# Kernel tuning notes

Hardware: AMD Instinct MI355X
Metric: run time of the kernel (lower is better)

Reference implementation:

```python
import jax, jax.numpy as jnp
from jax import lax
import numpy as np

B, H, W, D_MODEL = 2, 64, 64, 192
D_INNER, D_STATE, DT_RANK = 384, 16, 12
L = H * W
LN_EPS = 1e-5


def setup_inputs() -> dict:
    ks = jax.random.split(jax.random.key(0), 12)
    rng = np.random.default_rng(0)
    perm = rng.permutation(L).astype(np.int32)

    def p(i, shape, scale=0.02):
        return jax.random.normal(ks[i], shape, dtype=jnp.float32) * scale

    return {
        "x": jax.random.normal(ks[0], (B, H, W, D_MODEL), dtype=jnp.float32),
        "condition": jax.random.normal(ks[1], (B, H, W, D_MODEL), dtype=jnp.float32),
        "W_in": p(2, (2 * D_INNER, D_MODEL)),
        "W_con": p(3, (D_INNER, D_MODEL)),
        "conv_w": p(4, (D_INNER, 1, 3, 3)),
        "conv_b": jnp.zeros((D_INNER,), jnp.float32),
        "con_conv_w": p(5, (D_INNER, 1, 3, 3)),
        "con_conv_b": jnp.zeros((D_INNER,), jnp.float32),
        "x_proj_w": p(6, (DT_RANK + 2 * D_STATE, D_INNER)),
        "dt_proj_w": p(7, (D_INNER, DT_RANK)),
        "dt_proj_b": p(8, (D_INNER,), 0.1),
        "A_logs": jnp.tile(jnp.log(jnp.arange(1, D_STATE + 1, dtype=jnp.float32))[None, :], (D_INNER, 1)),
        "Ds": jnp.ones((D_INNER,), jnp.float32),
        "ln_w": jnp.ones((D_INNER,), jnp.float32),
        "ln_b": jnp.zeros((D_INNER,), jnp.float32),
        "W_out": p(9, (D_MODEL, D_INNER)),
        "scan_path": jnp.asarray(perm),
        "rev_scan_path": jnp.asarray(np.argsort(perm).astype(np.int32)),
    }


def _dwconv(x, w, b):
    # depthwise 3x3 conv, SAME padding; x: [B, C, H, W], w: [C, 1, 3, 3]
    y = lax.conv_general_dilated(x, w, (1, 1), "SAME",
                                 dimension_numbers=("NCHW", "OIHW", "NCHW"),
                                 feature_group_count=x.shape[1])
    return y + b[None, :, None, None]


def _selective_scan(u, delta, A, Bs, Cs, D):
    # u, delta: [B, D, L]; A: [D, N]; Bs, Cs: [B, N, L]; D: [D]
    dA = jnp.exp(jnp.einsum("bdl,dn->lbdn", delta, A))          # [L, B, D, N]
    dBu = jnp.einsum("bdl,bnl,bdl->lbdn", delta, Bs, u)          # [L, B, D, N]
    Ct = jnp.transpose(Cs, (2, 0, 1))                             # [L, B, N]
    h0 = jnp.zeros(dA.shape[1:], dA.dtype)

    def step(h, inp):
        a, b, c = inp
        h = a * h + b
        return h, jnp.einsum("bdn,bn->bd", h, c)

    _, ys = lax.scan(step, h0, (dA, dBu, Ct))                     # ys: [L, B, D]
    y = jnp.transpose(ys, (1, 2, 0))                              # [B, D, L]
    return y + u * D[None, :, None]


def _forward(x, condition, W_in, W_con, conv_w, conv_b, con_conv_w, con_conv_b,
             x_proj_w, dt_proj_w, dt_proj_b, A_logs, Ds, ln_w, ln_b, W_out,
             scan_path, rev_scan_path):
    b, h, w, _ = x.shape
    l = h * w
    xz = x @ W_in.T                                               # [B, H, W, 2*Din]
    xa, z = jnp.split(xz, 2, axis=-1)
    z = jax.nn.silu(z)
    c = condition @ W_con.T
    xa = jax.nn.silu(_dwconv(jnp.transpose(xa, (0, 3, 1, 2)), conv_w, conv_b))
    c = jax.nn.silu(_dwconv(jnp.transpose(c, (0, 3, 1, 2)), con_conv_w, con_conv_b))
    d = xa.shape[1]
    xs = xa.reshape(b, d, l)[:, :, scan_path]                     # forward_permutation, K=1
    cs = c.reshape(b, d, l)[:, :, scan_path]
    x_dbl = jnp.einsum("bdl,cd->bcl", xs + cs, x_proj_w)          # [B, R+2N, L]
    r, n = dt_proj_w.shape[1], A_logs.shape[1]
    dts = jnp.einsum("brl,dr->bdl", x_dbl[:, :r], dt_proj_w)
    Bs = x_dbl[:, r:r + n]
    Cs = x_dbl[:, r + n:]
    A = -jnp.exp(A_logs)
    delta = jax.nn.softplus(dts + dt_proj_b[None, :, None])       # delta_softplus=True
    y = _selective_scan(xs, delta, A, Bs, Cs, Ds)                 # [B, D, L]
    y = y[:, :, rev_scan_path]                                    # backward_permutation
    y = jnp.transpose(y, (0, 2, 1))                               # [B, L, D]
    mu = jnp.mean(y, axis=-1, keepdims=True)
    var = jnp.var(y, axis=-1, keepdims=True)
    y = (y - mu) * lax.rsqrt(var + LN_EPS) * ln_w + ln_b          # out_norm
    y = y.reshape(b, h, w, d) * z
    return y @ W_out.T                                            # out_proj (no bias)


def reference(x, condition, W_in, W_con, conv_w, conv_b, con_conv_w, con_conv_b,
              x_proj_w, dt_proj_w, dt_proj_b, A_logs, Ds, ln_w, ln_b, W_out,
              scan_path, rev_scan_path):
    return _forward(x, condition, W_in, W_con, conv_w, conv_b, con_conv_w,
                    con_conv_b, x_proj_w, dt_proj_w, dt_proj_b, A_logs, Ds,
                    ln_w, ln_b, W_out, scan_path, rev_scan_path)
```

## Files before the change

### kernel.cpp

```cpp
#include <hip/hip_runtime.h>
#include <math.h>

#define BB 2
#define HH 64
#define WW 64
#define DM 192
#define DI 384
#define NS 16
#define DTR 12
#define LL 4096
#define ROWS (BB*LL)
#define NCHUNK 64
#define LCHUNK 64
#define NCOMB 448

typedef __attribute__((ext_vector_type(8))) short bf16x8;
typedef __attribute__((ext_vector_type(4))) float f32x4;

__device__ __forceinline__ float silu_f(float v) {
    return v / (1.0f + __expf(-v));
}

__device__ __forceinline__ unsigned short f2bf(float f) {
    union { float f; unsigned int u; } c; c.f = f;
    unsigned int u = c.u;
    u += 0x7fffu + ((u >> 16) & 1u);
    return (unsigned short)(u >> 16);
}

__global__ __launch_bounds__(256) void cast_bf16(
    const float* __restrict__ in, unsigned short* __restrict__ out, int n4)
{
    int i = blockIdx.x * 256 + threadIdx.x;
    if (i >= n4) return;
    float4 v = ((const float4*)in)[i];
    ushort4 o;
    o.x = f2bf(v.x); o.y = f2bf(v.y); o.z = f2bf(v.z); o.w = f2bf(v.w);
    ((ushort4*)out)[i] = o;
}

__global__ __launch_bounds__(256) void cast_weights(
    const float* __restrict__ w_in, const float* __restrict__ w_con,
    const float* __restrict__ w_out,
    unsigned short* __restrict__ w_in_bf, unsigned short* __restrict__ w_con_bf,
    unsigned short* __restrict__ w_out_bf)
{
    int i = blockIdx.x * 256 + threadIdx.x;
    if (i >= 73728) return;
    const float4* src; ushort4* dst; int off;
    if (i < 36864)      { src = (const float4*)w_in;  dst = (ushort4*)w_in_bf;  off = i; }
    else if (i < 55296) { src = (const float4*)w_con; dst = (ushort4*)w_con_bf; off = i - 36864; }
    else                { src = (const float4*)w_out; dst = (ushort4*)w_out_bf; off = i - 55296; }
    float4 v = src[off];
    ushort4 o;
    o.x = f2bf(v.x); o.y = f2bf(v.y); o.z = f2bf(v.z); o.w = f2bf(v.w);
    dst[off] = o;
}

__global__ __launch_bounds__(256) void make_wcomb(
    const float* __restrict__ x_proj_w,
    const float* __restrict__ dt_w,
    unsigned short* __restrict__ wc)
{
    int idx = blockIdx.x * 256 + threadIdx.x;
    if (idx >= NCOMB * DI) return;
    int row = idx / DI, k = idx - row * DI;
    float v = 0.f;
    if (row < 384) {
        const float* dw = dt_w + row * DTR;
        #pragma unroll
        for (int r = 0; r < DTR; ++r) v += dw[r] * x_proj_w[r * DI + k];
    } else if (row < 416) {
        v = x_proj_w[(12 + (row - 384)) * DI + k];
    }
    wc[idx] = f2bf(v);
}

__device__ __forceinline__ void gemm_epilogue(
    int mode, int row, int col, int N, float v,
    const float* __restrict__ bias,
    float* __restrict__ out0, float* __restrict__ out1)
{
    if (mode == 0) {
        if (col < 384) out0[(size_t)row * 384 + col] = v;
        else           out1[(size_t)row * 384 + (col - 384)] = silu_f(v);
    } else if (mode == 1) {
        out0[(size_t)row * N + col] = v;
    } else {
        if (col < 384) {
            float a = v + bias[col];
            out0[(size_t)row * 384 + col] = (a > 20.f) ? a : log1pf(__expf(a));
        } else if (col < 416) {
            int idx = col - 384;
            int pos = (idx < 16) ? ((idx & 7) * 4 + (idx >> 3))
                                 : (((idx - 16) & 7) * 4 + 2 + ((idx - 16) >> 3));
            out1[(size_t)row * 32 + pos] = v;
        }
    }
}

__global__ __launch_bounds__(256) void gemm_bf16(
    const unsigned short* __restrict__ A, const unsigned short* __restrict__ W,
    const float* __restrict__ bias,
    float* __restrict__ out0, float* __restrict__ out1,
    int M, int N, int K, int mode)
{
    __shared__ __align__(16) unsigned short sA[64 * 40];
    __shared__ __align__(16) unsigned short sB[64 * 40];
    const int bm = blockIdx.x * 64;
    const int bn = blockIdx.y * 64;
    const int tid  = threadIdx.x;
    const int wave = tid >> 6;
    const int lane = tid & 63;
    const int quad = lane >> 4;
    const int l16  = lane & 15;

    const int lrow = tid >> 2;
    const int lkof = (tid & 3) * 8;

    f32x4 acc[4];
    #pragma unroll
    for (int t = 0; t < 4; ++t) acc[t] = (f32x4)(0.f);

    const int arow = (wave * 16 + l16) * 40 + quad * 8;

    for (int k0 = 0; k0 < K; k0 += 32) {
        *(bf16x8*)&sA[lrow * 40 + lkof] =
            *(const bf16x8*)&A[(size_t)(bm + lrow) * K + k0 + lkof];
        *(bf16x8*)&sB[lrow * 40 + lkof] =
            *(const bf16x8*)&W[(size_t)(bn + lrow) * K + k0 + lkof];
        __syncthreads();
        bf16x8 a = *(bf16x8*)&sA[arow];
        #pragma unroll
        for (int t = 0; t < 4; ++t) {
            bf16x8 b = *(bf16x8*)&sB[(t * 16 + l16) * 40 + quad * 8];
            acc[t] = __builtin_amdgcn_mfma_f32_16x16x32_bf16(a, b, acc[t], 0, 0, 0);
        }
        __syncthreads();
    }

    #pragma unroll
    for (int t = 0; t < 4; ++t) {
        int col = bn + t * 16 + l16;
        #pragma unroll
        for (int r = 0; r < 4; ++r) {
            int row = bm + wave * 16 + quad * 4 + r;
            gemm_epilogue(mode, row, col, N, acc[t][r], bias, out0, out1);
        }
    }
}

__global__ __launch_bounds__(256) void dwconv2_scatter(
    const float* __restrict__ xin, const float* __restrict__ cin,
    const float* __restrict__ wx, const float* __restrict__ bx,
    const float* __restrict__ wc, const float* __restrict__ bc,
    const int* __restrict__ rev_scan_path,
    float* __restrict__ xs_buf, unsigned short* __restrict__ s_bf)
{
    const int tile = blockIdx.x;
    const int c0   = blockIdx.y * 64;
    const int b    = blockIdx.z;
    const int h0 = (tile >> 3) * 8, w0 = (tile & 7) * 8;
    __shared__ float smx[10 * 10 * 64];
    __shared__ float smc[10 * 10 * 64];
    __shared__ int   jtile[64];

    for (int idx = threadIdx.x; idx < 6400; idx += 256) {
        int pix = idx >> 6, ch = idx & 63;
        int py = pix / 10, px = pix - py * 10;
        int gh = h0 + py - 1, gw = w0 + px - 1;
        float vx = 0.f, vc = 0.f;
        if (gh >= 0 && gh < 64 && gw >= 0 && gw < 64) {
            size_t g = ((size_t)(b * LL + gh * 64 + gw)) * DI + c0 + ch;
            vx = xin[g]; vc = cin[g];
        }
        smx[idx] = vx; smc[idx] = vc;
    }
    if (threadIdx.x < 64) {
        int l = (h0 + (threadIdx.x >> 3)) * 64 + (w0 + (threadIdx.x & 7));
        jtile[threadIdx.x] = rev_scan_path[l];
    }
    __syncthreads();

    const int ch = threadIdx.x & 63;
    const int pq = threadIdx.x >> 6;
    float wrx[9], wrc[9];
    #pragma unroll
    for (int k = 0; k < 9; ++k) {
        wrx[k] = wx[(c0 + ch) * 9 + k];
        wrc[k] = wc[(c0 + ch) * 9 + k];
    }
    const float bvx = bx[c0 + ch];
    const float bvc = bc[c0 + ch];

    #pragma unroll
    for (int i = 0; i < 16; ++i) {
        int p  = pq * 16 + i;
        int ph = p >> 3, pw = p & 7;
        float ax = bvx, ac = bvc;
        #pragma unroll
        for (int ki = 0; ki < 3; ++ki)
            #pragma unroll
            for (int kj = 0; kj < 3; ++kj) {
                int si = ((ph + ki) * 10 + (pw + kj)) * 64 + ch;
                ax += wrx[ki * 3 + kj] * smx[si];
                ac += wrc[ki * 3 + kj] * smc[si];
            }
        float xv = silu_f(ax);
        float sv = xv + silu_f(ac);
        size_t o = ((size_t)(b * LL + jtile[p])) * DI + c0 + ch;
        xs_buf[o] = xv;
        s_bf[o]   = f2bf(sv);
    }
}

__global__ __launch_bounds__(256) void scan_chunkA(
    const float* __restrict__ xs, const float* __restrict__ delta,
    const float* __restrict__ btct, const float* __restrict__ A_logs,
    float* __restrict__ chunkA, float* __restrict__ chunkB)
{
    const int c = blockIdx.x;
    const int g = blockIdx.y;
    const int b = blockIdx.z;
    const int t = threadIdx.x;
    const int grp = t >> 3, p = t & 7;
    const int d = g * 32 + grp;
    const float Av0 = -__expf(A_logs[d * NS + p]);
    const float Av1 = -__expf(A_logs[d * NS + p + 8]);
    const int j0 = c * LCHUNK;

    const float*  dl = delta + ((size_t)b * LL + j0) * DI + d;
    const float*  ul = xs    + ((size_t)b * LL + j0) * DI + d;
    const float2* bl = (const float2*)btct + ((size_t)b * LL + j0) * 16 + p * 2;

    float h0 = 0.f, h1 = 0.f, P0 = 1.f, P1 = 1.f;
    float dv[4], uv[4]; float2 bv[4];
    #pragma unroll
    for (int q = 0; q < 4; ++q) {
        dv[q] = dl[(size_t)q * DI]; uv[q] = ul[(size_t)q * DI]; bv[q] = bl[(size_t)q * 16];
    }
    for (int j = 0; j < LCHUNK; j += 4) {
        float nd[4], nu[4]; float2 nb[4];
        if (j + 4 < LCHUNK) {
            #pragma unroll
            for (int q = 0; q < 4; ++q) {
                int jj = j + 4 + q;
                nd[q] = dl[(size_t)jj * DI]; nu[q] = ul[(size_t)jj * DI]; nb[q] = bl[(size_t)jj * 16];
            }
        }
        #pragma unroll
        for (int q = 0; q < 4; ++q) {
            float e0 = __expf(dv[q] * Av0);
            float e1 = __expf(dv[q] * Av1);
            float du = dv[q] * uv[q];
            h0 = e0 * h0 + bv[q].x * du;
            h1 = e1 * h1 + bv[q].y * du;
            P0 *= e0; P1 *= e1;
        }
        #pragma unroll
        for (int q = 0; q < 4; ++q) { dv[q]=nd[q]; uv[q]=nu[q]; bv[q]=nb[q]; }
    }
    size_t idx = (((size_t)c * BB + b) * DI + d) * 8 + p;
    ((float2*)chunkA)[idx] = make_float2(P0, P1);
    ((float2*)chunkB)[idx] = make_float2(h0, h1);
}

__global__ __launch_bounds__(256) void scan_combine(
    const float* __restrict__ chunkA, const float* __restrict__ chunkB,
    float* __restrict__ hstart)
{
    const int gid = blockIdx.x * 256 + threadIdx.x;
    const size_t stride = (size_t)BB * DI * NS;
    float h = 0.f;
    float a = chunkA[gid], bv = chunkB[gid];
    for (int c = 0; c < NCHUNK; ++c) {
        float na = 0.f, nb = 0.f;
        if (c + 1 < NCHUNK) {
            na = chunkA[(size_t)(c + 1) * stride + gid];
            nb = chunkB[(size_t)(c + 1) * stride + gid];
        }
        hstart[(size_t)c * stride + gid] = h;
        h = a * h + bv;
        a = na; bv = nb;
    }
}

__global__ __launch_bounds__(256) void scan_chunkC(
    const float* __restrict__ xs, const float* __restrict__ delta,
    const float* __restrict__ btct,
    const float* __restrict__ A_logs, const float* __restrict__ Ds,
    const float* __restrict__ hstart,
    float* __restrict__ yt)
{
    const int c = blockIdx.x;
    const int g = blockIdx.y;
    const int b = blockIdx.z;
    const int t = threadIdx.x;
    const int grp = t >> 3, p = t & 7;
    const int d = g * 32 + grp;
    const float Av0 = -__expf(A_logs[d * NS + p]);
    const float Av1 = -__expf(A_logs[d * NS + p + 8]);
    const float Dv = Ds[d];
    const int j0 = c * LCHUNK;

    const float*  dl  = delta + ((size_t)b * LL + j0) * DI + d;
    const float*  ul  = xs    + ((size_t)b * LL + j0) * DI + d;
    const float4* bcl = (const float4*)btct + ((size_t)b * LL + j0) * 8 + p;
    float* yl = yt + ((size_t)b * LL + j0) * DI + d;

    float2 h = ((const float2*)hstart)[(((size_t)c * BB + b) * DI + d) * 8 + p];
    float h0 = h.x, h1 = h.y;

    float dv[4], uv[4]; float4 bc[4];
    #pragma unroll
    for (int q = 0; q < 4; ++q) {
        dv[q] = dl[(size_t)q * DI]; uv[q] = ul[(size_t)q * DI]; bc[q] = bcl[(size_t)q * 8];
    }
    for (int j = 0; j < LCHUNK; j += 4) {
        float nd[4], nu[4]; float4 nbc[4];
        if (j + 4 < LCHUNK) {
            #pragma unroll
            for (int q = 0; q < 4; ++q) {
                int jj = j + 4 + q;
                nd[q] = dl[(size_t)jj * DI]; nu[q] = ul[(size_t)jj * DI]; nbc[q] = bcl[(size_t)jj * 8];
            }
        }
        #pragma unroll
        for (int q = 0; q < 4; ++q) {
            float e0 = __expf(dv[q] * Av0);
            float e1 = __expf(dv[q] * Av1);
            float du = dv[q] * uv[q];
            h0 = e0 * h0 + bc[q].x * du;
            h1 = e1 * h1 + bc[q].y * du;
            float acc = h0 * bc[q].z + h1 * bc[q].w;
            acc += __shfl_xor(acc, 4, 8);
            acc += __shfl_xor(acc, 2, 8);
            acc += __shfl_xor(acc, 1, 8);
            if (p == 0) yl[(size_t)(j + q) * DI] = acc + uv[q] * Dv;
        }
        #pragma unroll
        for (int q = 0; q < 4; ++q) { dv[q]=nd[q]; uv[q]=nu[q]; bc[q]=nbc[q]; }
    }
}

__global__ __launch_bounds__(128) void ln_mul(
    const float* __restrict__ yt, const float* __restrict__ z,
    const int* __restrict__ scan_path,
    const float* __restrict__ ln_w, const float* __restrict__ ln_b,
    unsigned short* __restrict__ yn)
{
    const int j = blockIdx.x;
    const int b = blockIdx.y;
    const int l = scan_path[j];
    const int t = threadIdx.x;
    const float* row = yt + ((size_t)(b * LL + j)) * DI;
    float v0 = row[t], v1 = row[t + 128], v2 = row[t + 256];
    float s  = v0 + v1 + v2;
    float s2 = v0*v0 + v1*v1 + v2*v2;
    #pragma unroll
    for (int off = 32; off > 0; off >>= 1) {
        s  += __shfl_down(s, off);
        s2 += __shfl_down(s2, off);
    }
    __shared__ float red[4];
    if ((t & 63) == 0) { red[(t >> 6) * 2] = s; red[(t >> 6) * 2 + 1] = s2; }
    __syncthreads();
    float S  = red[0] + red[2];
    float S2 = red[1] + red[3];
    float mu  = S * (1.0f / DI);
    float var = S2 * (1.0f / DI) - mu * mu;
    float inv = rsqrtf(var + 1e-5f);

    const float* zr = z + ((size_t)(b * LL + l)) * DI;
    unsigned short* o = yn + ((size_t)(b * LL + l)) * DI;
    o[t]       = f2bf(((v0 - mu) * inv * ln_w[t]       + ln_b[t])       * zr[t]);
    o[t + 128] = f2bf(((v1 - mu) * inv * ln_w[t + 128] + ln_b[t + 128]) * zr[t + 128]);
    o[t + 256] = f2bf(((v2 - mu) * inv * ln_w[t + 256] + ln_b[t + 256]) * zr[t + 256]);
}

extern "C" void kernel_launch(void* const* d_in, const int* in_sizes, int n_in,
                              void* d_out, int out_size, void* d_ws, size_t ws_size,
                              hipStream_t stream) {
    const float* x          = (const float*)d_in[0];
    const float* cond       = (const float*)d_in[1];
    const float* W_in       = (const float*)d_in[2];
    const float* W_con      = (const float*)d_in[3];
    const float* conv_w     = (const float*)d_in[4];
    const float* conv_b     = (const float*)d_in[5];
    const float* con_conv_w = (const float*)d_in[6];
    const float* con_conv_b = (const float*)d_in[7];
    const float* x_proj_w   = (const float*)d_in[8];
    const float* dt_proj_w  = (const float*)d_in[9];
    const float* dt_proj_b  = (const float*)d_in[10];
    const float* A_logs     = (const float*)d_in[11];
    const float* Ds         = (const float*)d_in[12];
    const float* ln_w       = (const float*)d_in[13];
    const float* ln_b       = (const float*)d_in[14];
    const float* W_out      = (const float*)d_in[15];
    const int*   scan_path  = (const int*)d_in[16];
    const int*   rev_path   = (const int*)d_in[17];

    float* ws = (float*)d_ws;
    const size_t S  = (size_t)BB * LL * DI;
    const size_t SC = (size_t)NCHUNK * BB * DI * NS;
    float* xa_pre  = ws + 0 * S;
    float* z_silu  = ws + 1 * S;
    float* c_pre   = ws + 2 * S;
    float* xs_buf  = ws + 3 * S;
    float* dl_buf  = ws + 4 * S;
    float* btct    = ws + 5 * S;
    float* chunkA  = btct + (size_t)BB * LL * 32;
    float* chunkB  = chunkA + SC;
    float* hstart  = chunkB + SC;
    float* bfpool  = hstart + SC;

    unsigned short* x_bf    = (unsigned short*)bfpool;
    unsigned short* c_bf    = x_bf + (size_t)ROWS * DM;
    unsigned short* s_bf    = x_bf;
    unsigned short* w_in_bf  = c_bf + (size_t)ROWS * DM;
    unsigned short* w_con_bf = w_in_bf + 768 * DM;
    unsigned short* w_out_bf = w_con_bf + 384 * DM;
    unsigned short* wcomb_bf = w_out_bf + 192 * DI;
    unsigned short* yn_bf    = (unsigned short*)c_pre;
    float* yt = xa_pre;

    cast_bf16<<<(ROWS * DM / 4 + 255) / 256, 256, 0, stream>>>(x, x_bf, ROWS * DM / 4);
    cast_bf16<<<(ROWS * DM / 4 + 255) / 256, 256, 0, stream>>>(cond, c_bf, ROWS * DM / 4);
    cast_weights<<<(73728 + 255) / 256, 256, 0, stream>>>(
        W_in, W_con, W_out, w_in_bf, w_con_bf, w_out_bf);
    make_wcomb<<<(NCOMB * DI + 255) / 256, 256, 0, stream>>>(x_proj_w, dt_proj_w, wcomb_bf);

    gemm_bf16<<<dim3(ROWS / 64, 768 / 64), 256, 0, stream>>>(
        x_bf, w_in_bf, nullptr, xa_pre, z_silu, ROWS, 768, DM, 0);
    gemm_bf16<<<dim3(ROWS / 64, 384 / 64), 256, 0, stream>>>(
        c_bf, w_con_bf, nullptr, c_pre, nullptr, ROWS, 384, DM, 1);
    dwconv2_scatter<<<dim3(64, 6, BB), 256, 0, stream>>>(
        xa_pre, c_pre, conv_w, conv_b, con_conv_w, con_conv_b,
        rev_path, xs_buf, s_bf);
    gemm_bf16<<<dim3(ROWS / 64, NCOMB / 64), 256, 0, stream>>>(
        s_bf, wcomb_bf, dt_proj_b, dl_buf, btct, ROWS, NCOMB, DI, 2);
    scan_chunkA<<<dim3(NCHUNK, DI / 32, BB), 256, 0, stream>>>(
        xs_buf, dl_buf, btct, A_logs, chunkA, chunkB);
    scan_combine<<<(BB * DI * NS) / 256, 256, 0, stream>>>(chunkA, chunkB, hstart);
    scan_chunkC<<<dim3(NCHUNK, DI / 32, BB), 256, 0, stream>>>(
        xs_buf, dl_buf, btct, A_logs, Ds, hstart, yt);
    ln_mul<<<dim3(LL, BB), 128, 0, stream>>>(yt, z_silu, scan_path, ln_w, ln_b, yn_bf);
    gemm_bf16<<<dim3(ROWS / 64, 192 / 64), 256, 0, stream>>>(
        yn_bf, w_out_bf, nullptr, (float*)d_out, nullptr, ROWS, DM, DI, 1);
}
```

Before: 231.0 us.

## Fuse casts into GEMMs, LayerNorm into out-proj, and restructure chunk scan combine

Folds the activation bf16 casts into a single dual GEMM that converts fp32 inputs while loading tiles, and merges the three weight-prep kernels into one launch. The chunk decay product is replaced by exp(sum(delta)*A), and the chunk state layout becomes chunk-contiguous per (b,d,p) so each combine thread walks float2 pairs sequentially. LayerNorm, z-gating and the gather via rev_path are fused into the output projection GEMM, removing the yn intermediate buffer and one launch. The change trades intermediate traffic and launches for heavier per-block work, and the gathered LN rows now use the reverse permutation rather than scattering through scan_path.

```diff
diff --git a/kernel.cpp b/kernel.cpp
--- a/kernel.cpp
+++ b/kernel.cpp
@@ -28,52 +28,46 @@
     return (unsigned short)(u >> 16);
 }
 
-__global__ __launch_bounds__(256) void cast_bf16(
-    const float* __restrict__ in, unsigned short* __restrict__ out, int n4)
-{
-    int i = blockIdx.x * 256 + threadIdx.x;
-    if (i >= n4) return;
-    float4 v = ((const float4*)in)[i];
-    ushort4 o;
-    o.x = f2bf(v.x); o.y = f2bf(v.y); o.z = f2bf(v.z); o.w = f2bf(v.w);
-    ((ushort4*)out)[i] = o;
-}
-
-__global__ __launch_bounds__(256) void cast_weights(
+__device__ __forceinline__ bf16x8 f2bf8(float4 a, float4 b) {
+    bf16x8 r;
+    r[0] = (short)f2bf(a.x); r[1] = (short)f2bf(a.y);
+    r[2] = (short)f2bf(a.z); r[3] = (short)f2bf(a.w);
+    r[4] = (short)f2bf(b.x); r[5] = (short)f2bf(b.y);
+    r[6] = (short)f2bf(b.z); r[7] = (short)f2bf(b.w);
+    return r;
+}
+
+__global__ __launch_bounds__(256) void prep_weights(
     const float* __restrict__ w_in, const float* __restrict__ w_con,
     const float* __restrict__ w_out,
+    const float* __restrict__ x_proj_w, const float* __restrict__ dt_w,
     unsigned short* __restrict__ w_in_bf, unsigned short* __restrict__ w_con_bf,
-    unsigned short* __restrict__ w_out_bf)
-{
-    int i = blockIdx.x * 256 + threadIdx.x;
-    if (i >= 73728) return;
-    const float4* src; ushort4* dst; int off;
-    if (i < 36864)      { src = (const float4*)w_in;  dst = (ushort4*)w_in_bf;  off = i; }
-    else if (i < 55296) { src = (const float4*)w_con; dst = (ushort4*)w_con_bf; off = i - 36864; }
-    else                { src = (const float4*)w_out; dst = (ushort4*)w_out_bf; off = i - 55296; }
-    float4 v = src[off];
-    ushort4 o;
-    o.x = f2bf(v.x); o.y = f2bf(v.y); o.z = f2bf(v.z); o.w = f2bf(v.w);
-    dst[off] = o;
-}
-
-__global__ __launch_bounds__(256) void make_wcomb(
-    const float* __restrict__ x_proj_w,
-    const float* __restrict__ dt_w,
-    unsigned short* __restrict__ wc)
+    unsigned short* __restrict__ w_out_bf, unsigned short* __restrict__ wc)
 {
     int idx = blockIdx.x * 256 + threadIdx.x;
-    if (idx >= NCOMB * DI) return;
-    int row = idx / DI, k = idx - row * DI;
-    float v = 0.f;
-    if (row < 384) {
-        const float* dw = dt_w + row * DTR;
-        #pragma unroll
-        for (int r = 0; r < DTR; ++r) v += dw[r] * x_proj_w[r * DI + k];
-    } else if (row < 416) {
-        v = x_proj_w[(12 + (row - 384)) * DI + k];
-    }
-    wc[idx] = f2bf(v);
+    if (idx < 73728) {
+        const float4* src; ushort4* dst; int off;
+        if (idx < 36864)      { src = (const float4*)w_in;  dst = (ushort4*)w_in_bf;  off = idx; }
+        else if (idx < 55296) { src = (const float4*)w_con; dst = (ushort4*)w_con_bf; off = idx - 36864; }
+        else                  { src = (const float4*)w_out; dst = (ushort4*)w_out_bf; off = idx - 55296; }
+        float4 v = src[off];
+        ushort4 o;
+        o.x = f2bf(v.x); o.y = f2bf(v.y); o.z = f2bf(v.z); o.w = f2bf(v.w);
+        dst[off] = o;
+    } else {
+        int e = idx - 73728;
+        if (e >= NCOMB * DI) return;
+        int row = e / DI, k = e - row * DI;
+        float v = 0.f;
+        if (row < 384) {
+            const float* dw = dt_w + row * DTR;
+            #pragma unroll
+            for (int r = 0; r < DTR; ++r) v += dw[r] * x_proj_w[r * DI + k];
+        } else if (row < 416) {
+            v = x_proj_w[(12 + (row - 384)) * DI + k];
+        }
+        wc[e] = f2bf(v);
+    }
 }
 
 __device__ __forceinline__ void gemm_epilogue(
@@ -114,7 +108,6 @@
     const int lane = tid & 63;
     const int quad = lane >> 4;
     const int l16  = lane & 15;
-
     const int lrow = tid >> 2;
     const int lkof = (tid & 3) * 8;
 
@@ -146,6 +139,68 @@
         for (int r = 0; r < 4; ++r) {
             int row = bm + wave * 16 + quad * 4 + r;
             gemm_epilogue(mode, row, col, N, acc[t][r], bias, out0, out1);
+        }
+    }
+}
+
+__global__ __launch_bounds__(256) void gemm_dual(
+    const float* __restrict__ x, const float* __restrict__ cond,
+    const unsigned short* __restrict__ w_in_bf,
+    const unsigned short* __restrict__ w_con_bf,
+    float* __restrict__ xa_pre, float* __restrict__ z_silu,
+    float* __restrict__ c_pre)
+{
+    const int zz = blockIdx.z;
+    if (zz == 1 && blockIdx.y >= 6) return;
+    const float* A = zz ? cond : x;
+    const unsigned short* W = zz ? w_con_bf : w_in_bf;
+    float* out0 = zz ? c_pre : xa_pre;
+    float* out1 = z_silu;
+    const int mode = zz ? 1 : 0;
+    const int N = zz ? 384 : 768;
+
+    __shared__ __align__(16) unsigned short sA[64 * 40];
+    __shared__ __align__(16) unsigned short sB[64 * 40];
+    const int bm = blockIdx.x * 64;
+    const int bn = blockIdx.y * 64;
+    const int tid  = threadIdx.x;
+    const int wave = tid >> 6;
+    const int lane = tid & 63;
+    const int quad = lane >> 4;
+    const int l16  = lane & 15;
+    const int lrow = tid >> 2;
+    const int lkof = (tid & 3) * 8;
+
+    f32x4 acc[4];
+    #pragma unroll
+    for (int t = 0; t < 4; ++t) acc[t] = (f32x4)(0.f);
+
+    const int arow = (wave * 16 + l16) * 40 + quad * 8;
+
+    for (int k0 = 0; k0 < DM; k0 += 32) {
+        const float* ap = &A[(size_t)(bm + lrow) * DM + k0 + lkof];
+        float4 a0 = *(const float4*)ap;
+        float4 a1 = *(const float4*)(ap + 4);
+        *(bf16x8*)&sA[lrow * 40 + lkof] = f2bf8(a0, a1);
+        *(bf16x8*)&sB[lrow * 40 + lkof] =
+            *(const bf16x8*)&W[(size_t)(bn + lrow) * DM + k0 + lkof];
+        __syncthreads();
+        bf16x8 a = *(bf16x8*)&sA[arow];
+        #pragma unroll
+        for (int t = 0; t < 4; ++t) {
+            bf16x8 b = *(bf16x8*)&sB[(t * 16 + l16) * 40 + quad * 8];
+            acc[t] = __builtin_amdgcn_mfma_f32_16x16x32_bf16(a, b, acc[t], 0, 0, 0);
+        }
+        __syncthreads();
+    }
+
+    #pragma unroll
+    for (int t = 0; t < 4; ++t) {
+        int col = bn + t * 16 + l16;
+        #pragma unroll
+        for (int r = 0; r < 4; ++r) {
+            int row = bm + wave * 16 + quad * 4 + r;
+            gemm_epilogue(mode, row, col, N, acc[t][r], nullptr, out0, out1);
         }
     }
 }
@@ -233,7 +288,7 @@
     const float*  ul = xs    + ((size_t)b * LL + j0) * DI + d;
     const float2* bl = (const float2*)btct + ((size_t)b * LL + j0) * 16 + p * 2;
 
-    float h0 = 0.f, h1 = 0.f, P0 = 1.f, P1 = 1.f;
+    float h0 = 0.f, h1 = 0.f, Sd = 0.f;
     float dv[4], uv[4]; float2 bv[4];
     #pragma unroll
     for (int q = 0; q < 4; ++q) {
@@ -255,13 +310,13 @@
             float du = dv[q] * uv[q];
             h0 = e0 * h0 + bv[q].x * du;
             h1 = e1 * h1 + bv[q].y * du;
-            P0 *= e0; P1 *= e1;
+            Sd += dv[q];
         }
         #pragma unroll
         for (int q = 0; q < 4; ++q) { dv[q]=nd[q]; uv[q]=nu[q]; bv[q]=nb[q]; }
     }
-    size_t idx = (((size_t)c * BB + b) * DI + d) * 8 + p;
-    ((float2*)chunkA)[idx] = make_float2(P0, P1);
+    size_t idx = (((size_t)b * DI + d) * 8 + p) * NCHUNK + c;
+    ((float2*)chunkA)[idx] = make_float2(__expf(Sd * Av0), __expf(Sd * Av1));
     ((float2*)chunkB)[idx] = make_float2(h0, h1);
 }
 
@@ -270,18 +325,15 @@
     float* __restrict__ hstart)
 {
     const int gid = blockIdx.x * 256 + threadIdx.x;
-    const size_t stride = (size_t)BB * DI * NS;
-    float h = 0.f;
-    float a = chunkA[gid], bv = chunkB[gid];
+    const float2* A2 = (const float2*)chunkA + (size_t)gid * NCHUNK;
+    const float2* B2 = (const float2*)chunkB + (size_t)gid * NCHUNK;
+    float2*       H2 = (float2*)hstart       + (size_t)gid * NCHUNK;
+    float h0 = 0.f, h1 = 0.f;
     for (int c = 0; c < NCHUNK; ++c) {
-        float na = 0.f, nb = 0.f;
-        if (c + 1 < NCHUNK) {
-            na = chunkA[(size_t)(c + 1) * stride + gid];
-            nb = chunkB[(size_t)(c + 1) * stride + gid];
-        }
-        hstart[(size_t)c * stride + gid] = h;
-        h = a * h + bv;
-        a = na; bv = nb;
+        float2 a = A2[c], bv = B2[c];
+        H2[c] = make_float2(h0, h1);
+        h0 = a.x * h0 + bv.x;
+        h1 = a.y * h1 + bv.y;
     }
 }
 
@@ -308,7 +360,7 @@
     const float4* bcl = (const float4*)btct + ((size_t)b * LL + j0) * 8 + p;
     float* yl = yt + ((size_t)b * LL + j0) * DI + d;
 
-    float2 h = ((const float2*)hstart)[(((size_t)c * BB + b) * DI + d) * 8 + p];
+    float2 h = ((const float2*)hstart)[(((size_t)b * DI + d) * 8 + p) * NCHUNK + c];
     float h0 = h.x, h1 = h.y;
 
     float dv[4], uv[4]; float4 bc[4];
@@ -343,39 +395,88 @@
     }
 }
 
-__global__ __launch_bounds__(128) void ln_mul(
+__global__ __launch_bounds__(256) void ln_gemm(
     const float* __restrict__ yt, const float* __restrict__ z,
-    const int* __restrict__ scan_path,
+    const int* __restrict__ rev_path,
     const float* __restrict__ ln_w, const float* __restrict__ ln_b,
-    unsigned short* __restrict__ yn)
-{
-    const int j = blockIdx.x;
-    const int b = blockIdx.y;
-    const int l = scan_path[j];
-    const int t = threadIdx.x;
-    const float* row = yt + ((size_t)(b * LL + j)) * DI;
-    float v0 = row[t], v1 = row[t + 128], v2 = row[t + 256];
-    float s  = v0 + v1 + v2;
-    float s2 = v0*v0 + v1*v1 + v2*v2;
-    #pragma unroll
-    for (int off = 32; off > 0; off >>= 1) {
-        s  += __shfl_down(s, off);
-        s2 += __shfl_down(s2, off);
-    }
-    __shared__ float red[4];
-    if ((t & 63) == 0) { red[(t >> 6) * 2] = s; red[(t >> 6) * 2 + 1] = s2; }
+    const unsigned short* __restrict__ w_out_bf,
+    float* __restrict__ out)
+{
+    __shared__ __align__(16) unsigned short sA[32 * 392];
+    __shared__ __align__(16) unsigned short sB[192 * 40];
+    const int l0 = blockIdx.x * 32;
+    const int tid  = threadIdx.x;
+    const int wave = tid >> 6;
+    const int lane = tid & 63;
+
+    for (int r = wave; r < 32; r += 4) {
+        int gl = l0 + r;
+        int b = gl >> 12;
+        int pos = gl & (LL - 1);
+        int j = b * LL + rev_path[pos];
+        const float* yrow = yt + (size_t)j * DI;
+        float v[6];
+        float s = 0.f, s2 = 0.f;
+        #pragma unroll
+        for (int i = 0; i < 6; ++i) {
+            v[i] = yrow[lane + 64 * i];
+            s += v[i]; s2 += v[i] * v[i];
+        }
+        #pragma unroll
+        for (int off = 32; off > 0; off >>= 1) {
+            s  += __shfl_xor(s, off);
+            s2 += __shfl_xor(s2, off);
+        }
+        float mu  = s * (1.0f / DI);
+        float var = s2 * (1.0f / DI) - mu * mu;
+        float inv = rsqrtf(var + 1e-5f);
+        const float* zrow = z + (size_t)gl * DI;
+        #pragma unroll
+        for (int i = 0; i < 6; ++i) {
+            int cidx = lane + 64 * i;
+            float val = ((v[i] - mu) * inv * ln_w[cidx] + ln_b[cidx]) * zrow[cidx];
+            sA[r * 392 + cidx] = f2bf(val);
+        }
+    }
     __syncthreads();
-    float S  = red[0] + red[2];
-    float S2 = red[1] + red[3];
-    float mu  = S * (1.0f / DI);
-    float var = S2 * (1.0f / DI) - mu * mu;
-    float inv = rsqrtf(var + 1e-5f);
-
-    const float* zr = z + ((size_t)(b * LL + l)) * DI;
-    unsigned short* o = yn + ((size_t)(b * LL + l)) * DI;
-    o[t]       = f2bf(((v0 - mu) * inv * ln_w[t]       + ln_b[t])       * zr[t]);
-    o[t + 128] = f2bf(((v1 - mu) * inv * ln_w[t + 128] + ln_b[t + 128]) * zr[t + 128]);
-    o[t + 256] = f2bf(((v2 - mu) * inv * ln_w[t + 256] + ln_b[t + 256]) * zr[t + 256]);
+
+    const int quad = lane >> 4;
+    const int l16  = lane & 15;
+    const int wr  = wave >> 1;
+    const int wc2 = wave & 1;
+    const int r2  = tid >> 2;
+    const int kof = (tid & 3) * 8;
+
+    f32x4 acc[6];
+    #pragma unroll
+    for (int cI = 0; cI < 6; ++cI) acc[cI] = (f32x4)(0.f);
+
+    for (int k0 = 0; k0 < DI; k0 += 32) {
+        #pragma unroll
+        for (int it = 0; it < 3; ++it) {
+            int row = r2 + it * 64;
+            *(bf16x8*)&sB[row * 40 + kof] =
+                *(const bf16x8*)&w_out_bf[(size_t)row * DI + k0 + kof];
+        }
+        __syncthreads();
+        bf16x8 a = *(bf16x8*)&sA[(wr * 16 + l16) * 392 + k0 + quad * 8];
+        #pragma unroll
+        for (int cI = 0; cI < 6; ++cI) {
+            bf16x8 bb = *(bf16x8*)&sB[(wc2 * 96 + cI * 16 + l16) * 40 + quad * 8];
+            acc[cI] = __builtin_amdgcn_mfma_f32_16x16x32_bf16(a, bb, acc[cI], 0, 0, 0);
+        }
+        __syncthreads();
+    }
+
+    #pragma unroll
+    for (int cI = 0; cI < 6; ++cI) {
+        int col = wc2 * 96 + cI * 16 + l16;
+        #pragma unroll
+        for (int r = 0; r < 4; ++r) {
+            int row = l0 + wr * 16 + quad * 4 + r;
+            out[(size_t)row * DM + col] = acc[cI][r];
+        }
+    }
 }
 
 extern "C" void kernel_launch(void* const* d_in, const int* in_sizes, int n_in,
@@ -399,6 +500,7 @@
     const float* W_out      = (const float*)d_in[15];
     const int*   scan_path  = (const int*)d_in[16];
     const int*   rev_path   = (const int*)d_in[17];
+    (void)scan_path;
 
     float* ws = (float*)d_ws;
     const size_t S  = (size_t)BB * LL * DI;
@@ -414,26 +516,19 @@
     float* hstart  = chunkB + SC;
     float* bfpool  = hstart + SC;
 
-    unsigned short* x_bf    = (unsigned short*)bfpool;
-    unsigned short* c_bf    = x_bf + (size_t)ROWS * DM;
-    unsigned short* s_bf    = x_bf;
-    unsigned short* w_in_bf  = c_bf + (size_t)ROWS * DM;
+    unsigned short* s_bf     = (unsigned short*)bfpool;
+    unsigned short* w_in_bf  = s_bf + (size_t)ROWS * DI;
     unsigned short* w_con_bf = w_in_bf + 768 * DM;
     unsigned short* w_out_bf = w_con_bf + 384 * DM;
     unsigned short* wcomb_bf = w_out_bf + 192 * DI;
-    unsigned short* yn_bf    = (unsigned short*)c_pre;
     float* yt = xa_pre;
 
-    cast_bf16<<<(ROWS * DM / 4 + 255) / 256, 256, 0, stream>>>(x, x_bf, ROWS * DM / 4);
-    cast_bf16<<<(ROWS * DM / 4 + 255) / 256, 256, 0, stream>>>(cond, c_bf, ROWS * DM / 4);
-    cast_weights<<<(73728 + 255) / 256, 256, 0, stream>>>(
-        W_in, W_con, W_out, w_in_bf, w_con_bf, w_out_bf);
-    make_wcomb<<<(NCOMB * DI + 255) / 256, 256, 0, stream>>>(x_proj_w, dt_proj_w, wcomb_bf);
-
-    gemm_bf16<<<dim3(ROWS / 64, 768 / 64), 256, 0, stream>>>(
-        x_bf, w_in_bf, nullptr, xa_pre, z_silu, ROWS, 768, DM, 0);
-    gemm_bf16<<<dim3(ROWS / 64, 384 / 64), 256, 0, stream>>>(
-        c_bf, w_con_bf, nullptr, c_pre, nullptr, ROWS, 384, DM, 1);
+    prep_weights<<<(73728 + NCOMB * DI + 255) / 256, 256, 0, stream>>>(
+        W_in, W_con, W_out, x_proj_w, dt_proj_w,
+        w_in_bf, w_con_bf, w_out_bf, wcomb_bf);
+
+    gemm_dual<<<dim3(ROWS / 64, 12, 2), 256, 0, stream>>>(
+        x, cond, w_in_bf, w_con_bf, xa_pre, z_silu, c_pre);
     dwconv2_scatter<<<dim3(64, 6, BB), 256, 0, stream>>>(
         xa_pre, c_pre, conv_w, conv_b, con_conv_w, con_conv_b,
         rev_path, xs_buf, s_bf);
@@ -441,10 +536,9 @@
         s_bf, wcomb_bf, dt_proj_b, dl_buf, btct, ROWS, NCOMB, DI, 2);
     scan_chunkA<<<dim3(NCHUNK, DI / 32, BB), 256, 0, stream>>>(
         xs_buf, dl_buf, btct, A_logs, chunkA, chunkB);
-    scan_combine<<<(BB * DI * NS) / 256, 256, 0, stream>>>(chunkA, chunkB, hstart);
+    scan_combine<<<(BB * DI * 8) / 256, 256, 0, stream>>>(chunkA, chunkB, hstart);
     scan_chunkC<<<dim3(NCHUNK, DI / 32, BB), 256, 0, stream>>>(
         xs_buf, dl_buf, btct, A_logs, Ds, hstart, yt);
-    ln_mul<<<dim3(LL, BB), 128, 0, stream>>>(yt, z_silu, scan_path, ln_w, ln_b, yn_bf);
-    gemm_bf16<<<dim3(ROWS / 64, 192 / 64), 256, 0, stream>>>(
-        yn_bf, w_out_bf, nullptr, (float*)d_out, nullptr, ROWS, DM, DI, 1);
-}
+    ln_gemm<<<ROWS / 32, 256, 0, stream>>>(
+        yt, z_silu, rev_path, ln_w, ln_b, w_out_bf, (float*)d_out);
+}
```

Measured after the change: 238.1 us. 1.03x slower.
